# Performance work log

Hardware: AMD Instinct MI355X
Metric: run time of the kernel (lower is better)

Reference implementation:

```python
import jax, jax.numpy as jnp
import numpy as np

D = 1024
H = 16
DH = D // H  # 64
FF_H = 4096
EPS = 1e-5


def layernorm(x, gamma, beta):
    mu = jnp.mean(x, axis=-1, keepdims=True)
    var = jnp.var(x, axis=-1, keepdims=True)
    return (x - mu) * jax.lax.rsqrt(var + EPS) * gamma + beta


def setup_inputs() -> dict:
    key = jax.random.key(0)
    ks = jax.random.split(key, 12)
    B, S = 2, 2048
    q = jax.random.normal(ks[0], (B, S, D), dtype=jnp.float32)
    k = jax.random.normal(ks[1], (B, S, D), dtype=jnp.float32)
    v = jax.random.normal(ks[2], (B, S, D), dtype=jnp.float32)
    time_lengths = jax.random.randint(ks[3], (B,), 0, S)
    mask = jnp.zeros((1, 1, S, S), dtype=jnp.float32)
    sc = 0.02
    Wq = jax.random.normal(ks[4], (D, D), dtype=jnp.float32) * sc
    Wk = jax.random.normal(ks[5], (D, D), dtype=jnp.float32) * sc
    Wv = jax.random.normal(ks[6], (D, D), dtype=jnp.float32) * sc
    Wd = jax.random.normal(ks[7], (D, D), dtype=jnp.float32) * sc
    W1 = jax.random.normal(ks[8], (D, FF_H), dtype=jnp.float32) * sc
    b1 = jnp.zeros((FF_H,), dtype=jnp.float32)
    W2 = jax.random.normal(ks[9], (FF_H, D), dtype=jnp.float32) * sc
    b2 = jnp.zeros((D,), dtype=jnp.float32)
    g1 = jnp.ones((D,), dtype=jnp.float32)
    be1 = jnp.zeros((D,), dtype=jnp.float32)
    g2 = jnp.ones((D,), dtype=jnp.float32)
    be2 = jnp.zeros((D,), dtype=jnp.float32)
    return {"q": q, "k": k, "v": v, "time_lengths": time_lengths, "mask": mask,
            "Wq": Wq, "Wk": Wk, "Wv": Wv, "Wd": Wd,
            "W1": W1, "b1": b1, "W2": W2, "b2": b2,
            "g1": g1, "be1": be1, "g2": g2, "be2": be2}


def reference(q, k, v, time_lengths, mask, Wq, Wk, Wv, Wd, W1, b1, W2, b2, g1, be1, g2, be2):
    B, S, _ = q.shape
    scale = jnp.sqrt(jnp.float32(DH))
    # project and split heads: [B,H,S,DH]
    qh = (q @ Wq).reshape(B, S, H, DH).transpose(0, 2, 1, 3)
    kh = (k @ Wk).reshape(B, S, H, DH).transpose(0, 2, 1, 3)
    vh = (v @ Wv).reshape(B, S, H, DH).transpose(0, 2, 1, 3)
    score = jnp.einsum('bhqd,bhkd->bhqk', qh, kh) / scale + mask
    attn = jax.nn.softmax(score, axis=-1)
    z = jnp.einsum('bhqk,bhkd->bhqd', attn, vh)
    z = z.transpose(0, 2, 1, 3).reshape(B, S, D)
    z = z @ Wd
    # Add & LayerNorm 1 (note: original applies LN to attn out, then adds q)
    x = layernorm(z, g1, be1) + q
    # FF (dropout is identity in eval)
    ff = jax.nn.relu(x @ W1 + b1) @ W2 + b2
    return layernorm(ff + x, g2, be2)
```

## Files before the change

### kernel.cpp

```cpp
#include <hip/hip_runtime.h>
#include <hip/hip_bf16.h>


#define SEQ 2048
#define DM  1024
#define LNEPS 1e-5f

typedef __attribute__((ext_vector_type(8))) short bf16x8;
typedef __attribute__((ext_vector_type(4))) float f32x4;

#define GAS __attribute__((address_space(1)))
#define LAS __attribute__((address_space(3)))

static __device__ __forceinline__ void gl_lds16(const unsigned short* g, unsigned short* l) {
    __builtin_amdgcn_global_load_lds((const GAS void*)g, (LAS void*)l, 16, 0, 0);
}

static __device__ __forceinline__ unsigned short f2bf(float f) {
    unsigned u = __builtin_bit_cast(unsigned, f);
    u += 0x7fffu + ((u >> 16) & 1u);
    return (unsigned short)(u >> 16);
}

static __device__ __forceinline__ unsigned cvt_pk_bf16(float lo, float hi) {
    unsigned r;
    asm("v_cvt_pk_bf16_f32 %0, %1, %2" : "=v"(r) : "v"(lo), "v"(hi));
    return r;
}

__global__ __launch_bounds__(256) void gemm_bf16(
    const unsigned short* __restrict__ A, const unsigned short* __restrict__ Bt,
    float* __restrict__ Cf, unsigned short* __restrict__ Cb,
    unsigned short* __restrict__ CbT,
    int M, int N, int Klen, int lda, int ldb,
    size_t sA, size_t sB, size_t sC,
    const float* __restrict__ bias, int ep, int lgn, int zskip)
{
    __shared__ unsigned short As[2][128 * 32];
    __shared__ unsigned short Bs[2][128 * 32];

    const int t = threadIdx.x, lane = t & 63, w = t >> 6;
    const int wm = w >> 1, wn = w & 1;

    const int nwg = gridDim.x;
    const int sw = (blockIdx.x & 7) * (nwg >> 3) + (blockIdx.x >> 3);
    const int n0 = (sw & ((1 << lgn) - 1)) * 128;
    const int m0 = (sw >> lgn) * 128;

    A  += (size_t)blockIdx.z * sA;
    Bt += (size_t)blockIdx.z * sB;
    int zi = blockIdx.z; if (zskip && zi >= 2) zi++;
    const size_t cbase = (size_t)zi * sC;
    const int l15 = lane & 15, l16 = lane >> 4;
    const int ar = lane >> 2, ac = (lane & 3) * 8;

    f32x4 acc[4][4];
    #pragma unroll
    for (int i = 0; i < 4; i++)
        #pragma unroll
        for (int j = 0; j < 4; j++)
            acc[i][j] = (f32x4){0.f, 0.f, 0.f, 0.f};

    auto stage = [&](int buf, int k0) {
        #pragma unroll
        for (int i = 0; i < 2; i++) {
            const int rg = w * 2 + i;
            gl_lds16(&A [(size_t)(m0 + rg * 16 + ar) * lda + k0 + ac], &As[buf][rg * 512]);
            gl_lds16(&Bt[(size_t)(n0 + rg * 16 + ar) * ldb + k0 + ac], &Bs[buf][rg * 512]);
        }
    };
    auto compute = [&](int buf) {
        bf16x8 af[4], bfr[4];
        #pragma unroll
        for (int i = 0; i < 4; i++) {
            af[i]  = *(const bf16x8*)&As[buf][(wm * 64 + i * 16 + l15) * 32 + l16 * 8];
            bfr[i] = *(const bf16x8*)&Bs[buf][(wn * 64 + i * 16 + l15) * 32 + l16 * 8];
        }
        #pragma unroll
        for (int mi = 0; mi < 4; mi++)
            #pragma unroll
            for (int ni = 0; ni < 4; ni++)
                acc[mi][ni] = __builtin_amdgcn_mfma_f32_16x16x32_bf16(
                    af[mi], bfr[ni], acc[mi][ni], 0, 0, 0);
    };

    stage(0, 0);
    __syncthreads();
    int k0 = 0;
    for (; k0 + 32 < Klen; k0 += 32) {
        const int cur = (k0 >> 5) & 1;
        stage(cur ^ 1, k0 + 32);
        compute(cur);
        __syncthreads();
    }
    compute((k0 >> 5) & 1);

    if (CbT && blockIdx.z == 2) {
        #pragma unroll
        for (int ni = 0; ni < 4; ni++) {
            const int col = n0 + wn * 64 + ni * 16 + l15;
            const int hh = col >> 6, d = col & 63;
            #pragma unroll
            for (int mi = 0; mi < 4; mi++) {
                const int row = m0 + wm * 64 + mi * 16 + l16 * 4;
                const int bb = row >> 11, s = row & 2047;
                ushort4 o;
                o.x = f2bf(acc[mi][ni][0]); o.y = f2bf(acc[mi][ni][1]);
                o.z = f2bf(acc[mi][ni][2]); o.w = f2bf(acc[mi][ni][3]);
                *(ushort4*)&CbT[((size_t)((bb * 16 + hh) * 64 + d)) * SEQ + s] = o;
            }
        }
        return;
    }

    #pragma unroll
    for (int ni = 0; ni < 4; ni++) {
        const int col = n0 + wn * 64 + ni * 16 + l15;
        const float bv = (ep && blockIdx.z == 0) ? bias[col] : 0.f;
        #pragma unroll
        for (int mi = 0; mi < 4; mi++) {
            #pragma unroll
            for (int r = 0; r < 4; r++) {
                const int row = m0 + wm * 64 + mi * 16 + l16 * 4 + r;
                float vv = acc[mi][ni][r] + bv;
                if (ep == 2) vv = fmaxf(vv, 0.f);
                if (Cf) Cf[cbase + (size_t)row * N + col] = vv;
                else    Cb[cbase + (size_t)row * N + col] = f2bf(vv);
            }
        }
    }
}

__global__ __launch_bounds__(256) void attn_mfma(
    const unsigned short* __restrict__ qh, const unsigned short* __restrict__ kh,
    const unsigned short* __restrict__ vhT, const float* __restrict__ mask,
    unsigned short* __restrict__ z)
{
    __shared__ unsigned short Ks0[64 * 64];
    __shared__ unsigned short Ks1[64 * 64];
    __shared__ unsigned short Vst[64 * 64];
    __shared__ unsigned short Ps[64 * 72];

    const int t = threadIdx.x, lane = t & 63, w = t >> 6;
    const int bid = blockIdx.x;
    const int qt = bid >> 5, h = bid & 15, b = (bid >> 4) & 1;
    const int q0 = qt * 64, qr = w * 16;
    const int l15 = lane & 15, l16 = lane >> 4;

    const int lr = lane >> 3;
    const int gc = ((lane & 7) ^ lr) * 8;

    const size_t qbase = (size_t)(b * SEQ + q0) * DM + h * 64;
    const size_t kbase = (size_t)(b * SEQ) * DM + h * 64;
    const size_t vbase = (size_t)((b * 16 + h) * 64) * SEQ;

    #pragma unroll
    for (int i = 0; i < 2; i++) {
        const int rg = w * 2 + i;
        gl_lds16(&qh[qbase + (size_t)(rg * 8 + lr) * DM + gc], &Ks1[rg * 512]);
        gl_lds16(&kh[kbase + (size_t)(rg * 8 + lr) * DM + gc], &Ks0[rg * 512]);
    }
    __syncthreads();

    const int sw0 = ((l16    ) ^ (l15 & 7)) * 8;
    const int sw1 = ((l16 + 4) ^ (l15 & 7)) * 8;
    const bf16x8 bQ0 = *(const bf16x8*)&Ks1[(qr + l15) * 64 + sw0];
    const bf16x8 bQ1 = *(const bf16x8*)&Ks1[(qr + l15) * 64 + sw1];
    __syncthreads();

    const float* mrow = mask + (size_t)(q0 + qr + l15) * SEQ;

    float m_i = -1e30f, l_i = 0.f;
    f32x4 o4[4];
    #pragma unroll
    for (int mi = 0; mi < 4; mi++) o4[mi] = (f32x4){0.f, 0.f, 0.f, 0.f};

    for (int kt = 0; kt < SEQ / 64; kt++) {
        const int k0 = kt * 64;
        const int kn = ((kt + 1) & (SEQ / 64 - 1)) * 64;
        unsigned short* Kcur = (kt & 1) ? Ks1 : Ks0;
        unsigned short* Knxt = (kt & 1) ? Ks0 : Ks1;

        __builtin_amdgcn_s_barrier();

        float4 mv[4];
        #pragma unroll
        for (int ki = 0; ki < 4; ki++)
            mv[ki] = *(const float4*)&mrow[k0 + ki * 16 + l16 * 4];

        #pragma unroll
        for (int i = 0; i < 2; i++) {
            const int rg = w * 2 + i;
            gl_lds16(&vhT[vbase + (size_t)(rg * 8 + lr) * SEQ + k0 + gc], &Vst[rg * 512]);
        }
        __builtin_amdgcn_sched_barrier(0);
        #pragma unroll
        for (int i = 0; i < 2; i++) {
            const int rg = w * 2 + i;
            gl_lds16(&kh[kbase + (size_t)(kn + rg * 8 + lr) * DM + gc], &Knxt[rg * 512]);
        }

        asm volatile("s_waitcnt vmcnt(8)" ::: "memory");
        __builtin_amdgcn_s_barrier();
        __builtin_amdgcn_sched_barrier(0);

        f32x4 s4[4];
        __builtin_amdgcn_s_setprio(1);
        #pragma unroll
        for (int ki = 0; ki < 4; ki++) {
            const int r = ki * 16 + l15;
            const bf16x8 aK0 = *(const bf16x8*)&Kcur[r * 64 + sw0];
            const bf16x8 aK1 = *(const bf16x8*)&Kcur[r * 64 + sw1];
            f32x4 a0 = (f32x4){0.f, 0.f, 0.f, 0.f};
            a0 = __builtin_amdgcn_mfma_f32_16x16x32_bf16(aK0, bQ0, a0, 0, 0, 0);
            s4[ki] = __builtin_amdgcn_mfma_f32_16x16x32_bf16(aK1, bQ1, a0, 0, 0, 0);
        }
        __builtin_amdgcn_s_setprio(0);

        float sv[16];
        #pragma unroll
        for (int ki = 0; ki < 4; ki++) {
            sv[ki * 4 + 0] = s4[ki][0] * 0.125f + mv[ki].x;
            sv[ki * 4 + 1] = s4[ki][1] * 0.125f + mv[ki].y;
            sv[ki * 4 + 2] = s4[ki][2] * 0.125f + mv[ki].z;
            sv[ki * 4 + 3] = s4[ki][3] * 0.125f + mv[ki].w;
        }

        float rm = fmaxf(sv[0], sv[1]);
        #pragma unroll
        for (int i = 2; i < 16; i += 2) rm = fmaxf(fmaxf(rm, sv[i]), sv[i + 1]);
        rm = fmaxf(rm, __shfl_xor(rm, 16));
        rm = fmaxf(rm, __shfl_xor(rm, 32));

        const bool skip = __all(rm <= m_i + 8.f);
        float mnew = m_i, alpha = 1.f;
        if (!skip) { mnew = fmaxf(m_i, rm); alpha = __expf(m_i - mnew); }

        float ps = 0.f;
        #pragma unroll
        for (int ki = 0; ki < 4; ki++) {
            const float p0 = __expf(sv[ki * 4 + 0] - mnew);
            const float p1 = __expf(sv[ki * 4 + 1] - mnew);
            const float p2 = __expf(sv[ki * 4 + 2] - mnew);
            const float p3 = __expf(sv[ki * 4 + 3] - mnew);
            ps += (p0 + p1) + (p2 + p3);
            uint2 pk;
            pk.x = cvt_pk_bf16(p0, p1);
            pk.y = cvt_pk_bf16(p2, p3);
            *(uint2*)&Ps[(qr + l15) * 72 + ki * 16 + l16 * 4] = pk;
        }
        ps += __shfl_xor(ps, 16);
        ps += __shfl_xor(ps, 32);
        if (!skip) {
            m_i = mnew;
            l_i = l_i * alpha + ps;
            #pragma unroll
            for (int mi = 0; mi < 4; mi++)
                #pragma unroll
                for (int r = 0; r < 4; r++) o4[mi][r] *= alpha;
        } else {
            l_i += ps;
        }

        asm volatile("s_waitcnt vmcnt(2)" ::: "memory");
        __builtin_amdgcn_s_barrier();
        __builtin_amdgcn_sched_barrier(0);

        const bf16x8 bP0 = *(const bf16x8*)&Ps[(qr + l15) * 72 + l16 * 8];
        const bf16x8 bP1 = *(const bf16x8*)&Ps[(qr + l15) * 72 + 32 + l16 * 8];
        __builtin_amdgcn_s_setprio(1);
        #pragma unroll
        for (int mi = 0; mi < 4; mi++) {
            const int r = mi * 16 + l15;
            const bf16x8 aV0 = *(const bf16x8*)&Vst[r * 64 + sw0];
            const bf16x8 aV1 = *(const bf16x8*)&Vst[r * 64 + sw1];
            o4[mi] = __builtin_amdgcn_mfma_f32_16x16x32_bf16(aV0, bP0, o4[mi], 0, 0, 0);
            o4[mi] = __builtin_amdgcn_mfma_f32_16x16x32_bf16(aV1, bP1, o4[mi], 0, 0, 0);
        }
        __builtin_amdgcn_s_setprio(0);
    }

    asm volatile("s_waitcnt vmcnt(0)" ::: "memory");

    const float inv = 1.f / l_i;
    #pragma unroll
    for (int mi = 0; mi < 4; mi++) {
        const float a0 = o4[mi][0] * inv, a1 = o4[mi][1] * inv;
        const float a2 = o4[mi][2] * inv, a3 = o4[mi][3] * inv;
        uint2 ov;
        ov.x = cvt_pk_bf16(a0, a1);
        ov.y = cvt_pk_bf16(a2, a3);
        *(uint2*)&z[(size_t)(b * SEQ + q0 + qr + l15) * DM + h * 64 + mi * 16 + l16 * 4] = ov;
    }
}

__global__ __launch_bounds__(256) void prep(
    const float* __restrict__ q, const float* __restrict__ k, const float* __restrict__ v,
    unsigned short* __restrict__ qb,
    const float* __restrict__ Wq, const float* __restrict__ Wk,
    const float* __restrict__ Wv, const float* __restrict__ Wd,
    const float* __restrict__ W1, const float* __restrict__ W2,
    unsigned short* __restrict__ Wqt, unsigned short* __restrict__ Wdt,
    unsigned short* __restrict__ W1t, unsigned short* __restrict__ W2t)
{
    const int z = blockIdx.z, t = threadIdx.x;
    const int flat = blockIdx.y * 64 + blockIdx.x;

    if (z < 3) {
        const float* src = z == 0 ? q : (z == 1 ? k : v);
        unsigned short* dst = qb + (size_t)z * ((size_t)SEQ * 2 * DM);
        const size_t base = (size_t)flat * 4096 + t * 4;
        #pragma unroll
        for (int i = 0; i < 4; i++) {
            const float4 w4 = *(const float4*)&src[base + i * 1024];
            ushort4 o; o.x = f2bf(w4.x); o.y = f2bf(w4.y); o.z = f2bf(w4.z); o.w = f2bf(w4.w);
            *(ushort4*)&dst[base + i * 1024] = o;
        }
        return;
    }

    __shared__ float ts[64][65];
    const float* W; unsigned short* Wt; int K, N, n0, k0;
    if (z < 7) {
        if (flat >= 256) return;
        W  = z == 3 ? Wq : z == 4 ? Wk : (z == 5 ? Wv : Wd);
        Wt = z == 3 ? Wqt : z == 4 ? Wqt + 1024 * 1024
           : z == 5 ? Wqt + 2 * 1024 * 1024 : Wdt;
        K = 1024; N = 1024;
        n0 = (flat & 15) * 64; k0 = (flat >> 4) * 64;
    } else if (z == 7) {
        W = W1; Wt = W1t; K = 1024; N = 4096;
        n0 = blockIdx.x * 64; k0 = blockIdx.y * 64;
    } else {
        W = W2; Wt = W2t; K = 4096; N = 1024;
        n0 = (flat & 15) * 64; k0 = (flat >> 4) * 64;
    }

    const int r = t >> 4, c4 = (t & 15) * 4;
    #pragma unroll
    for (int i = 0; i < 4; i++) {
        const float4 v4 = *(const float4*)&W[(size_t)(k0 + r + i * 16) * N + n0 + c4];
        ts[r + i * 16][c4 + 0] = v4.x; ts[r + i * 16][c4 + 1] = v4.y;
        ts[r + i * 16][c4 + 2] = v4.z; ts[r + i * 16][c4 + 3] = v4.w;
    }
    __syncthreads();
    #pragma unroll
    for (int i = 0; i < 4; i++) {
        const int n = r + i * 16;
        ushort4 o;
        o.x = f2bf(ts[c4 + 0][n]); o.y = f2bf(ts[c4 + 1][n]);
        o.z = f2bf(ts[c4 + 2][n]); o.w = f2bf(ts[c4 + 3][n]);
        *(ushort4*)&Wt[(size_t)(n0 + n) * K + k0 + c4] = o;
    }
}

__global__ __launch_bounds__(256) void ln_res(
    const float* __restrict__ a, const float* __restrict__ a2,
    const float* __restrict__ a3, const float* __restrict__ a4,
    const float* __restrict__ r,
    const float* __restrict__ g, const float* __restrict__ be,
    float* __restrict__ out, unsigned short* __restrict__ outb, int mode)
{
    __shared__ float redls[8];
    const int row = blockIdx.x, t = threadIdx.x;
    const size_t base = (size_t)row * DM;

    float vals[4], s = 0.f, sq = 0.f;
    #pragma unroll
    for (int i = 0; i < 4; i++) {
        const int c = t + 256 * i;
        float x = a[base + c];
        if (a2) x += a2[base + c];
        if (a3) x += a3[base + c];
        if (a4) x += a4[base + c];
        if (mode == 1) x += r[base + c];
        vals[i] = x; s += x; sq += x * x;
    }
    #pragma unroll
    for (int off = 32; off > 0; off >>= 1) { s += __shfl_down(s, off); sq += __shfl_down(sq, off); }
    if ((t & 63) == 0) { redls[t >> 6] = s; redls[4 + (t >> 6)] = sq; }
    __syncthreads();
    s  = redls[0] + redls[1] + redls[2] + redls[3];
    sq = redls[4] + redls[5] + redls[6] + redls[7];

    const float mu  = s * (1.f / 1024.f);
    const float var = sq * (1.f / 1024.f) - mu * mu;
    const float rs  = rsqrtf(var + LNEPS);
    #pragma unroll
    for (int i = 0; i < 4; i++) {
        const int c = t + 256 * i;
        float y = (vals[i] - mu) * rs * g[c] + be[c];
        if (mode == 0) y += r[base + c];
        out[base + c] = y;
        if (outb) outb[base + c] = f2bf(y);
    }
}

extern "C" void kernel_launch(void* const* d_in, const int* in_sizes, int n_in,
                              void* d_out, int out_size, void* d_ws, size_t ws_size,
                              hipStream_t stream)
{
    const float* q    = (const float*)d_in[0];
    const float* k    = (const float*)d_in[1];
    const float* v    = (const float*)d_in[2];
    const float* mask = (const float*)d_in[4];
    const float* Wq   = (const float*)d_in[5];
    const float* Wk   = (const float*)d_in[6];
    const float* Wv   = (const float*)d_in[7];
    const float* Wd   = (const float*)d_in[8];
    const float* W1   = (const float*)d_in[9];
    const float* b1   = (const float*)d_in[10];
    const float* W2   = (const float*)d_in[11];
    const float* b2   = (const float*)d_in[12];
    const float* g1   = (const float*)d_in[13];
    const float* be1  = (const float*)d_in[14];
    const float* g2   = (const float*)d_in[15];
    const float* be2  = (const float*)d_in[16];
    float* out = (float*)d_out;

    char* WS = (char*)d_ws;
    const size_t MiB = 1u << 20;
    const size_t ND  = (size_t)4096 * 1024;

    unsigned short* qb  = (unsigned short*)(WS + 0);
    unsigned short* zb  = (unsigned short*)(WS + 8 * MiB);
    unsigned short* xb  = (unsigned short*)(WS + 16 * MiB);
    unsigned short* Wqt = (unsigned short*)(WS + 24 * MiB);
    unsigned short* Wdt = (unsigned short*)(WS + 30 * MiB);
    unsigned short* W1t = (unsigned short*)(WS + 32 * MiB);
    unsigned short* W2t = (unsigned short*)(WS + 40 * MiB);
    unsigned short* qh  = (unsigned short*)(WS + 48 * MiB);
    unsigned short* vhT = (unsigned short*)(WS + 64 * MiB);
    float*          zd0 = (float*)(WS + 48 * MiB);
    float*          zd1 = (float*)(WS + 64 * MiB);
    float*          x   = (float*)(WS + 80 * MiB);
    unsigned short* h1  = (unsigned short*)(WS + 96 * MiB);
    float*          y0  = (float*)(WS + 0);
    float*          y1  = (float*)(WS + 16 * MiB);
    float*          y2  = (float*)(WS + 48 * MiB);
    float*          y3  = (float*)(WS + 64 * MiB);

    unsigned short* kh = qh + ND;

    const dim3 blk(256);

    prep<<<dim3(64, 16, 9), blk, 0, stream>>>(q, k, v, qb, Wq, Wk, Wv, Wd, W1, W2,
                                              Wqt, Wdt, W1t, W2t);

    gemm_bf16<<<dim3(256, 1, 3), blk, 0, stream>>>(qb, Wqt, nullptr, qh, vhT,
        4096, 1024, 1024, 1024, 1024, ND, (size_t)1024 * 1024, ND, nullptr, 0, 3, 0);

    attn_mfma<<<dim3(1024), blk, 0, stream>>>(qh, kh, vhT, mask, zb);

    gemm_bf16<<<dim3(256, 1, 2), blk, 0, stream>>>(zb, Wdt, zd0, nullptr, nullptr,
        4096, 1024, 512, 1024, 1024, 512, 512, ND, nullptr, 0, 3, 0);

    ln_res<<<dim3(4096), blk, 0, stream>>>(zd0, zd1, nullptr, nullptr, q,
                                           g1, be1, x, xb, 0);

    gemm_bf16<<<dim3(1024, 1, 1), blk, 0, stream>>>(xb, W1t, nullptr, h1, nullptr,
        4096, 4096, 1024, 1024, 1024, 0, 0, 0, b1, 2, 5, 0);
    gemm_bf16<<<dim3(256, 1, 4), blk, 0, stream>>>(h1, W2t, y0, nullptr, nullptr,
        4096, 1024, 1024, 4096, 4096, 1024, 1024, ND, b2, 1, 3, 1);

    ln_res<<<dim3(4096), blk, 0, stream>>>(y0, y1, y2, y3, x, g2, be2, out, nullptr, 1);
}
```

Baseline: 481.9 us.

## Add 256x256 tiled 8-wave GEMM for FF1 and halve FF2 split-K

Adds a new 512-thread GEMM kernel with 256x256 output tiles, 64-wide K steps, XOR-swizzled LDS, phased staging interleaved with MFMA groups, and a fused bias+ReLU bf16 epilogue, and uses it for the FF1 projection. The FF2 GEMM drops from 4-way to 2-way split-K, so the final layernorm sums two partials instead of four, and the zskip remapping is removed. The goal is more data reuse per tile and less partial-sum traffic, in exchange for fewer, heavier workgroups and higher LDS/register pressure.

```diff
diff --git a/kernel.cpp b/kernel.cpp
--- a/kernel.cpp
+++ b/kernel.cpp
@@ -26,6 +26,150 @@
     unsigned r;
     asm("v_cvt_pk_bf16_f32 %0, %1, %2" : "=v"(r) : "v"(lo), "v"(hi));
     return r;
+}
+
+__global__ __launch_bounds__(512) void gemm256(
+    const unsigned short* __restrict__ A, const unsigned short* __restrict__ Bt,
+    unsigned short* __restrict__ Cb,
+    int N, int Klen, int lda, int ldb,
+    const float* __restrict__ bias, int lgn)
+{
+    __shared__ unsigned short Asl[2][2][128 * 64];
+    __shared__ unsigned short Bsl[2][2][128 * 64];
+
+    const int t = threadIdx.x, lane = t & 63, w = t >> 6;
+    const int wm = w >> 2, wn = w & 3;
+    const int l15 = lane & 15, l16 = lane >> 4;
+
+    const int nwg = gridDim.x;
+    const int sw = (blockIdx.x & 7) * (nwg >> 3) + (blockIdx.x >> 3);
+    const int n0 = (sw & ((1 << lgn) - 1)) * 256;
+    const int m0 = (sw >> lgn) * 256;
+
+    const int sr = t >> 3, sc = t & 7;
+    const int gcs = (sc ^ (sr & 7)) * 8;
+
+    f32x4 acc[8][4];
+    #pragma unroll
+    for (int i = 0; i < 8; i++)
+        #pragma unroll
+        for (int j = 0; j < 4; j++)
+            acc[i][j] = (f32x4){0.f, 0.f, 0.f, 0.f};
+
+    auto STAGEPAIR = [&](int kt, int ph) {
+        const int slot = kt & 1;
+        if (ph < 2) {
+            #pragma unroll
+            for (int p = 0; p < 2; p++)
+                gl_lds16(&A[(size_t)(m0 + ph * 128 + p * 64 + sr) * lda + kt * 64 + gcs],
+                         &Asl[slot][ph][p * 4096 + w * 512]);
+        } else {
+            const int h = ph - 2;
+            #pragma unroll
+            for (int p = 0; p < 2; p++)
+                gl_lds16(&Bt[(size_t)(n0 + h * 128 + p * 64 + sr) * ldb + kt * 64 + gcs],
+                         &Bsl[slot][h][p * 4096 + w * 512]);
+        }
+    };
+
+    #pragma unroll
+    for (int ph = 0; ph < 4; ph++) STAGEPAIR(0, ph);
+
+    const int NT = Klen >> 6;
+    for (int T = 0; T < NT; T++) {
+        const int slot = T & 1;
+        const int Tn = (T + 1 < NT) ? T + 1 : 0;
+
+        bf16x8 afr[4][2], bfr[2][2];
+
+        auto LOADA = [&](int MH) {
+            #pragma unroll
+            for (int mi = 0; mi < 4; mi++)
+                #pragma unroll
+                for (int kk = 0; kk < 2; kk++) {
+                    const int r = MH * 64 + mi * 16 + l15;
+                    afr[mi][kk] = *(const bf16x8*)
+                        &Asl[slot][wm][r * 64 + (((kk * 4 + l16) ^ (r & 7)) * 8)];
+                }
+        };
+        auto LOADB = [&](int NH) {
+            #pragma unroll
+            for (int ni = 0; ni < 2; ni++)
+                #pragma unroll
+                for (int kk = 0; kk < 2; kk++) {
+                    const int r = (wn & 1) * 64 + NH * 32 + ni * 16 + l15;
+                    bfr[ni][kk] = *(const bf16x8*)
+                        &Bsl[slot][wn >> 1][r * 64 + (((kk * 4 + l16) ^ (r & 7)) * 8)];
+                }
+        };
+        auto MFMA16 = [&](int MH, int NH) {
+            __builtin_amdgcn_s_setprio(1);
+            #pragma unroll
+            for (int mi = 0; mi < 4; mi++)
+                #pragma unroll
+                for (int ni = 0; ni < 2; ni++) {
+                    acc[MH * 4 + mi][NH * 2 + ni] = __builtin_amdgcn_mfma_f32_16x16x32_bf16(
+                        afr[mi][0], bfr[ni][0], acc[MH * 4 + mi][NH * 2 + ni], 0, 0, 0);
+                    acc[MH * 4 + mi][NH * 2 + ni] = __builtin_amdgcn_mfma_f32_16x16x32_bf16(
+                        afr[mi][1], bfr[ni][1], acc[MH * 4 + mi][NH * 2 + ni], 0, 0, 0);
+                }
+            __builtin_amdgcn_s_setprio(0);
+        };
+
+        STAGEPAIR(Tn, 0);
+        asm volatile("s_waitcnt vmcnt(2)" ::: "memory");
+        __builtin_amdgcn_s_barrier();
+        __builtin_amdgcn_sched_barrier(0);
+        LOADA(0); LOADB(0);
+        asm volatile("s_waitcnt lgkmcnt(0)" ::: "memory");
+        __builtin_amdgcn_sched_barrier(0);
+        MFMA16(0, 0);
+        __builtin_amdgcn_s_barrier();
+
+        STAGEPAIR(Tn, 1);
+        __builtin_amdgcn_s_barrier();
+        __builtin_amdgcn_sched_barrier(0);
+        LOADB(1);
+        asm volatile("s_waitcnt lgkmcnt(0)" ::: "memory");
+        __builtin_amdgcn_sched_barrier(0);
+        MFMA16(0, 1);
+        __builtin_amdgcn_s_barrier();
+
+        STAGEPAIR(Tn, 2);
+        __builtin_amdgcn_s_barrier();
+        __builtin_amdgcn_sched_barrier(0);
+        LOADA(1);
+        asm volatile("s_waitcnt lgkmcnt(0)" ::: "memory");
+        __builtin_amdgcn_sched_barrier(0);
+        MFMA16(1, 1);
+        __builtin_amdgcn_s_barrier();
+
+        STAGEPAIR(Tn, 3);
+        __builtin_amdgcn_s_barrier();
+        __builtin_amdgcn_sched_barrier(0);
+        LOADB(0);
+        asm volatile("s_waitcnt lgkmcnt(0)" ::: "memory");
+        __builtin_amdgcn_sched_barrier(0);
+        MFMA16(1, 0);
+        __builtin_amdgcn_s_barrier();
+    }
+
+    asm volatile("s_waitcnt vmcnt(0)" ::: "memory");
+
+    #pragma unroll
+    for (int f = 0; f < 8; f++) {
+        const int row0 = m0 + wm * 128 + (f >> 2) * 64 + (f & 3) * 16 + l16 * 4;
+        #pragma unroll
+        for (int g = 0; g < 4; g++) {
+            const int col = n0 + wn * 64 + (g >> 1) * 32 + (g & 1) * 16 + l15;
+            const float bv = bias[col];
+            #pragma unroll
+            for (int r = 0; r < 4; r++) {
+                float vv = fmaxf(acc[f][g][r] + bv, 0.f);
+                Cb[(size_t)(row0 + r) * N + col] = f2bf(vv);
+            }
+        }
+    }
 }
 
 __global__ __launch_bounds__(256) void gemm_bf16(
@@ -34,7 +178,7 @@
     unsigned short* __restrict__ CbT,
     int M, int N, int Klen, int lda, int ldb,
     size_t sA, size_t sB, size_t sC,
-    const float* __restrict__ bias, int ep, int lgn, int zskip)
+    const float* __restrict__ bias, int ep, int lgn)
 {
     __shared__ unsigned short As[2][128 * 32];
     __shared__ unsigned short Bs[2][128 * 32];
@@ -49,8 +193,7 @@
 
     A  += (size_t)blockIdx.z * sA;
     Bt += (size_t)blockIdx.z * sB;
-    int zi = blockIdx.z; if (zskip && zi >= 2) zi++;
-    const size_t cbase = (size_t)zi * sC;
+    const size_t cbase = (size_t)blockIdx.z * sC;
     const int l15 = lane & 15, l16 = lane >> 4;
     const int ar = lane >> 2, ac = (lane & 3) * 8;
 
@@ -435,10 +578,8 @@
     float*          zd1 = (float*)(WS + 64 * MiB);
     float*          x   = (float*)(WS + 80 * MiB);
     unsigned short* h1  = (unsigned short*)(WS + 96 * MiB);
-    float*          y0  = (float*)(WS + 0);
-    float*          y1  = (float*)(WS + 16 * MiB);
-    float*          y2  = (float*)(WS + 48 * MiB);
-    float*          y3  = (float*)(WS + 64 * MiB);
+    float*          y0  = (float*)(WS + 48 * MiB);
+    float*          y1  = (float*)(WS + 64 * MiB);
 
     unsigned short* kh = qh + ND;
 
@@ -448,20 +589,22 @@
                                               Wqt, Wdt, W1t, W2t);
 
     gemm_bf16<<<dim3(256, 1, 3), blk, 0, stream>>>(qb, Wqt, nullptr, qh, vhT,
-        4096, 1024, 1024, 1024, 1024, ND, (size_t)1024 * 1024, ND, nullptr, 0, 3, 0);
+        4096, 1024, 1024, 1024, 1024, ND, (size_t)1024 * 1024, ND, nullptr, 0, 3);
 
     attn_mfma<<<dim3(1024), blk, 0, stream>>>(qh, kh, vhT, mask, zb);
 
     gemm_bf16<<<dim3(256, 1, 2), blk, 0, stream>>>(zb, Wdt, zd0, nullptr, nullptr,
-        4096, 1024, 512, 1024, 1024, 512, 512, ND, nullptr, 0, 3, 0);
+        4096, 1024, 512, 1024, 1024, 512, 512, ND, nullptr, 0, 3);
 
     ln_res<<<dim3(4096), blk, 0, stream>>>(zd0, zd1, nullptr, nullptr, q,
                                            g1, be1, x, xb, 0);
 
-    gemm_bf16<<<dim3(1024, 1, 1), blk, 0, stream>>>(xb, W1t, nullptr, h1, nullptr,
-        4096, 4096, 1024, 1024, 1024, 0, 0, 0, b1, 2, 5, 0);
-    gemm_bf16<<<dim3(256, 1, 4), blk, 0, stream>>>(h1, W2t, y0, nullptr, nullptr,
-        4096, 1024, 1024, 4096, 4096, 1024, 1024, ND, b2, 1, 3, 1);
-
-    ln_res<<<dim3(4096), blk, 0, stream>>>(y0, y1, y2, y3, x, g2, be2, out, nullptr, 1);
-}
+    gemm256<<<dim3(256), dim3(512), 0, stream>>>(xb, W1t, h1,
+        4096, 1024, 1024, 1024, b1, 4);
+
+    gemm_bf16<<<dim3(256, 1, 2), blk, 0, stream>>>(h1, W2t, y0, nullptr, nullptr,
+        4096, 1024, 2048, 4096, 4096, 2048, 2048, ND, b2, 1, 3);
+
+    ln_res<<<dim3(4096), blk, 0, stream>>>(y0, y1, nullptr, nullptr, x,
+                                           g2, be2, out, nullptr, 1);
+}
```

Measured after the change: 455.1 us. 5.6% less time.
